# Optimization experiments

Hardware: AMD Instinct MI355X
Metric: run time of the kernel (lower is better)

The kernel has to match this reference:

```python
import jax, jax.numpy as jnp
import numpy as np
from math import sqrt

BATCH = 32
NUM_CLASSES = 81   # incl. background (class 0 skipped)
MAX_DET = 200      # max_output / per-class NMS candidate cap
IOU_T = 0.5        # criteria in decode_batch_with_nms_trace
CONF_T = 0.05      # score mask threshold


def make_dboxes():
    """Replicates dboxes_R34_coco([1200,1200]) -> (15130, 4) xywh, clipped to [0,1]."""
    fig = 1200
    feat = [50, 25, 13, 7, 3, 3]
    scales = [int(s * fig / 300) for s in [21, 45, 99, 153, 207, 261, 315]]
    ars = [[2], [2, 3], [2, 3], [2, 3], [2], [2]]
    boxes = []
    for idx, f in enumerate(feat):
        sk1 = scales[idx] / fig
        sk2 = scales[idx + 1] / fig
        sk3 = sqrt(sk1 * sk2)
        sizes = [(sk1, sk1), (sk3, sk3)]
        for a in ars[idx]:
            w, h = sk1 * sqrt(a), sk1 / sqrt(a)
            sizes += [(w, h), (h, w)]
        fk = fig // (fig // f)
        for (w, h) in sizes:
            for i in range(f):
                for j in range(f):
                    boxes.append(((j + 0.5) / fk, (i + 0.5) / fk, w, h))
    return np.clip(np.asarray(boxes, np.float32), 0.0, 1.0)


def setup_inputs() -> dict:
    key = jax.random.key(0)
    k1, k2 = jax.random.split(key)
    db = make_dboxes()                      # (15130, 4)
    N = db.shape[0]
    return {
        "bboxes_in": jax.random.normal(k1, (BATCH, 4, N), jnp.float32),
        "scores_in": jax.random.normal(k2, (BATCH, NUM_CLASSES, N), jnp.float32),
        "scale_xy": jnp.full((1,), 0.1, jnp.float32),
        "scale_wh": jnp.full((1,), 0.2, jnp.float32),
        "dboxes_xywh": jnp.asarray(db)[None],  # (1, N, 4)
    }


def _scale_back(bboxes_in, scores_in, scale_xy, scale_wh, dboxes_xywh):
    bb = jnp.transpose(bboxes_in, (0, 2, 1))          # (B, N, 4)
    sc = jnp.transpose(scores_in, (0, 2, 1))          # (B, N, L)
    d_xy, d_wh = dboxes_xywh[..., :2], dboxes_xywh[..., 2:]
    xy = bb[..., :2] * scale_xy * d_wh + d_xy
    wh = jnp.exp(bb[..., 2:] * scale_wh) * d_wh
    ltrb = jnp.concatenate([xy - 0.5 * wh, xy + 0.5 * wh], axis=-1)
    return ltrb, jax.nn.softmax(sc, axis=-1)


def _pairwise_iou(a, b):
    lt = jnp.maximum(a[:, None, :2], b[None, :, :2])
    rb = jnp.minimum(a[:, None, 2:], b[None, :, 2:])
    wh = jnp.clip(rb - lt, 0.0)
    inter = wh[..., 0] * wh[..., 1]
    area_a = (a[:, 2] - a[:, 0]) * (a[:, 3] - a[:, 1])
    area_b = (b[:, 2] - b[:, 0]) * (b[:, 3] - b[:, 1])
    return inter / (area_a[:, None] + area_b[None, :] - inter)


def _nms_one_class(boxes, cls_scores):
    """boxes (N,4), cls_scores (N,) -> (MAX_DET,4), (MAX_DET,) with suppressed = -1."""
    s = jnp.where(cls_scores > CONF_T, cls_scores, -1.0)   # mask score > 0.05
    top_s, idx = jax.lax.top_k(s, MAX_DET)                 # descending topk
    b = boxes[idx]
    iou = _pairwise_iou(b, b)                              # (K, K)
    valid = top_s > CONF_T

    def body(i, keep):  # greedy NMS over score-sorted candidates
        sup = (iou[i] > IOU_T) & keep[i] & (jnp.arange(MAX_DET) > i)
        return keep & ~sup

    keep = jax.lax.stop_gradient(jax.lax.fori_loop(0, MAX_DET, body, valid))
    return b, jnp.where(keep, top_s, -1.0)


def _decode(bboxes_in, scores_in, scale_xy, scale_wh, dboxes_xywh):
    boxes, probs = _scale_back(bboxes_in, scores_in, scale_xy, scale_wh, dboxes_xywh)
    cls_scores = jnp.transpose(probs[..., 1:], (0, 2, 1))   # (B, C=80, N); skip bg
    B, C = cls_scores.shape[0], cls_scores.shape[1]
    per_class = jax.vmap(_nms_one_class, in_axes=(None, 0))
    kb, ks = jax.vmap(per_class, in_axes=(0, 0))(boxes, cls_scores)  # (B,C,K,4),(B,C,K)
    labels = jnp.broadcast_to(
        jnp.arange(1, C + 1, dtype=jnp.int32)[:, None], (C, MAX_DET)).reshape(-1)
    kb = kb.reshape(B, C * MAX_DET, 4)
    ks = ks.reshape(B, C * MAX_DET)
    top_s, top_i = jax.lax.top_k(ks, MAX_DET)               # global top-200
    fb = jnp.take_along_axis(kb, top_i[..., None], axis=1)  # (B, 200, 4)
    fl = labels[top_i]                                      # (B, 200)
    valid = top_s > CONF_T
    return (fb * valid[..., None].astype(fb.dtype),
            jnp.where(valid, fl, 0),
            jnp.where(valid, top_s, 0.0))


def reference(bboxes_in, scores_in, scale_xy, scale_wh, dboxes_xywh):
    return _decode(bboxes_in, scores_in, scale_xy, scale_wh, dboxes_xywh)
```

## Files before the change

### kernel.cpp

```cpp
#include <hip/hip_runtime.h>
#include <stdint.h>

#define NPRIOR   15130
#define BATCH    32
#define NCLS     81
#define NCLS_OUT 80
#define NDET     200
#define CONF_T   0.05f
#define IOU_T    0.5f
#define CAND_CAP 1024
#define NGRP     5
#define GRP      16

__global__ __launch_bounds__(256) void zero_counters(unsigned int* __restrict__ counters, int n) {
    int i = blockIdx.x * 256 + threadIdx.x;
    if (i < n) counters[i] = 0u;
}

__global__ __launch_bounds__(256) void decode_softmax_scatter(
    const float* __restrict__ bboxes,
    const float* __restrict__ scores,
    const float* __restrict__ scale_xy_p,
    const float* __restrict__ scale_wh_p,
    const float* __restrict__ dboxes,
    float* __restrict__ boxes_ltrb,
    unsigned int* __restrict__ counters,
    unsigned long long* __restrict__ cand_g)
{
    int b = blockIdx.y;
    int n = blockIdx.x * 256 + threadIdx.x;
    if (n >= NPRIOR) return;

    float sx = scale_xy_p[0], sw = scale_wh_p[0];
    const float* bb = bboxes + (size_t)b * 4 * NPRIOR + n;
    float bx = bb[0];
    float by = bb[NPRIOR];
    float bw = bb[2 * NPRIOR];
    float bh = bb[3 * NPRIOR];
    float dx = dboxes[n * 4 + 0], dy = dboxes[n * 4 + 1];
    float dw = dboxes[n * 4 + 2], dh = dboxes[n * 4 + 3];
    float x = __fadd_rn(__fmul_rn(__fmul_rn(bx, sx), dw), dx);
    float y = __fadd_rn(__fmul_rn(__fmul_rn(by, sx), dh), dy);
    float w = __fmul_rn(expf(__fmul_rn(bw, sw)), dw);
    float h = __fmul_rn(expf(__fmul_rn(bh, sw)), dh);
    float hw = __fmul_rn(0.5f, w), hh = __fmul_rn(0.5f, h);
    float4 box;
    box.x = __fsub_rn(x, hw);
    box.y = __fsub_rn(y, hh);
    box.z = __fadd_rn(x, hw);
    box.w = __fadd_rn(y, hh);
    ((float4*)boxes_ltrb)[(size_t)b * NPRIOR + n] = box;

    const float* sc = scores + (size_t)b * NCLS * NPRIOR + n;
    float v[NCLS];
    float mx = -INFINITY;
#pragma unroll
    for (int c = 0; c < NCLS; ++c) {
        v[c] = sc[(size_t)c * NPRIOR];
        mx = fmaxf(mx, v[c]);
    }
    float sum = 0.f;
#pragma unroll
    for (int c = 0; c < NCLS; ++c) {
        v[c] = expf(__fsub_rn(v[c], mx));
        sum = __fadd_rn(sum, v[c]);
    }

    unsigned int invn = 0xFFFFFFFFu - (unsigned int)n;
#pragma unroll
    for (int c = 1; c < NCLS; ++c) {
        float p = __fdiv_rn(v[c], sum);
        if (p > CONF_T) {
            unsigned int idx = (unsigned int)b * NCLS_OUT + (unsigned int)(c - 1);
            unsigned int pos = atomicAdd(&counters[idx], 1u);
            if (pos < CAND_CAP) {
                cand_g[(size_t)idx * CAND_CAP + pos] =
                    ((unsigned long long)__float_as_uint(p) << 32) | (unsigned long long)invn;
            }
        }
    }
}

__device__ inline void bitonic_desc(unsigned long long* keys, int P, int tid) {
    for (int k = 2; k <= P; k <<= 1) {
        for (int j = k >> 1; j > 0; j >>= 1) {
            for (int i = tid; i < P; i += 256) {
                int l = i ^ j;
                if (l > i) {
                    unsigned long long a = keys[i], b = keys[l];
                    bool desc = ((i & k) == 0);
                    if (desc ? (a < b) : (a > b)) {
                        keys[i] = b;
                        keys[l] = a;
                    }
                }
            }
            __syncthreads();
        }
    }
}

__global__ __launch_bounds__(256) void nms_class(
    const unsigned int* __restrict__ counters,
    const unsigned long long* __restrict__ cand_g,
    const float* __restrict__ boxes_ltrb,
    float* __restrict__ cls_scores,
    float* __restrict__ cls_boxes)
{
    __shared__ unsigned long long cand[CAND_CAP];
    __shared__ float sbox[NDET][4];
    __shared__ float sscore[NDET];
    __shared__ unsigned long long rowm[NDET][4];
    __shared__ unsigned long long keepw[4];

    int tid = threadIdx.x;
    int b = blockIdx.y;
    int bc = b * NCLS_OUT + blockIdx.x;

    unsigned int cntu = counters[bc];
    int cnt = (cntu > CAND_CAP) ? CAND_CAP : (int)cntu;

    int P = 256;
    while (P < cnt) P <<= 1;

    for (int i = tid; i < P; i += 256)
        cand[i] = (i < cnt) ? cand_g[(size_t)bc * CAND_CAP + i] : 0ull;
    __syncthreads();

    bitonic_desc(cand, P, tid);

    int m = cnt < NDET ? cnt : NDET;
    if (tid < m) {
        unsigned long long key = cand[tid];
        unsigned int n = 0xFFFFFFFFu - (unsigned int)(key & 0xFFFFFFFFull);
        sscore[tid] = __uint_as_float((unsigned int)(key >> 32));
        float4 bx = ((const float4*)boxes_ltrb)[(size_t)b * NPRIOR + n];
        sbox[tid][0] = bx.x;
        sbox[tid][1] = bx.y;
        sbox[tid][2] = bx.z;
        sbox[tid][3] = bx.w;
    }
    __syncthreads();

    if (tid < m) {
        float l0 = sbox[tid][0], t0 = sbox[tid][1], r0 = sbox[tid][2], b0 = sbox[tid][3];
        float area0 = __fmul_rn(__fsub_rn(r0, l0), __fsub_rn(b0, t0));
        unsigned long long w0 = 0, w1 = 0, w2 = 0, w3 = 0;
        for (int j = tid + 1; j < m; ++j) {
            float lj = sbox[j][0], tj = sbox[j][1], rj = sbox[j][2], bj = sbox[j][3];
            float ltx = fmaxf(l0, lj), lty = fmaxf(t0, tj);
            float rbx = fminf(r0, rj), rby = fminf(b0, bj);
            float iw = fmaxf(__fsub_rn(rbx, ltx), 0.f);
            float ih = fmaxf(__fsub_rn(rby, lty), 0.f);
            float inter = __fmul_rn(iw, ih);
            float areaj = __fmul_rn(__fsub_rn(rj, lj), __fsub_rn(bj, tj));
            float den = __fsub_rn(__fadd_rn(area0, areaj), inter);
            float iou = __fdiv_rn(inter, den);
            if (iou > IOU_T) {
                if (j < 64) w0 |= 1ull << j;
                else if (j < 128) w1 |= 1ull << (j - 64);
                else if (j < 192) w2 |= 1ull << (j - 128);
                else w3 |= 1ull << (j - 192);
            }
        }
        rowm[tid][0] = w0;
        rowm[tid][1] = w1;
        rowm[tid][2] = w2;
        rowm[tid][3] = w3;
    }
    __syncthreads();

    if (tid == 0) {
        auto maskf = [](int t) -> unsigned long long {
            if (t <= 0) return 0ull;
            if (t >= 64) return ~0ull;
            return (1ull << t) - 1ull;
        };
        unsigned long long k0 = maskf(m), k1 = maskf(m - 64), k2 = maskf(m - 128), k3 = maskf(m - 192);
        for (int i = 0; i < m; ++i) {
            unsigned long long cur = (i < 64) ? k0 : (i < 128) ? k1 : (i < 192) ? k2 : k3;
            if ((cur >> (i & 63)) & 1ull) {
                k0 &= ~rowm[i][0];
                k1 &= ~rowm[i][1];
                k2 &= ~rowm[i][2];
                k3 &= ~rowm[i][3];
            }
        }
        keepw[0] = k0; keepw[1] = k1; keepw[2] = k2; keepw[3] = k3;
    }
    __syncthreads();

    if (tid < NDET) {
        float s = -1.0f;
        if (tid < m && ((keepw[tid >> 6] >> (tid & 63)) & 1ull)) s = sscore[tid];
        cls_scores[(size_t)bc * NDET + tid] = s;
        if (tid < m) {
            float4 bx;
            bx.x = sbox[tid][0]; bx.y = sbox[tid][1];
            bx.z = sbox[tid][2]; bx.w = sbox[tid][3];
            ((float4*)cls_boxes)[(size_t)bc * NDET + tid] = bx;
        }
    }
}

__global__ __launch_bounds__(256) void topk_group(
    const float* __restrict__ cls_scores,
    unsigned long long* __restrict__ grp_keys)
{
    __shared__ unsigned long long keys[4096];
    __shared__ unsigned int cnt_s;

    int tid = threadIdx.x;
    int g = blockIdx.x, b = blockIdx.y;
    if (tid == 0) cnt_s = 0;
    __syncthreads();

    int base_e = g * GRP * NDET;
    const float* sp = cls_scores + (size_t)b * NCLS_OUT * NDET + base_e;
    for (int i = tid; i < GRP * NDET; i += 256) {
        float s = sp[i];
        if (s > CONF_T) {
            unsigned int pos = atomicAdd(&cnt_s, 1u);
            unsigned int e = (unsigned int)(base_e + i);
            keys[pos] = ((unsigned long long)__float_as_uint(s) << 32) |
                        (unsigned long long)(0xFFFFFFFFu - e);
        }
    }
    __syncthreads();
    int cnt = (int)cnt_s;
    int P = 256;
    while (P < cnt) P <<= 1;
    for (int i = tid; i < P; i += 256)
        if (i >= cnt) keys[i] = 0ull;
    __syncthreads();

    bitonic_desc(keys, P, tid);

    if (tid < NDET)
        grp_keys[((size_t)b * NGRP + g) * NDET + tid] = (tid < cnt) ? keys[tid] : 0ull;
}

__global__ __launch_bounds__(256) void final_topk(
    const unsigned long long* __restrict__ grp_keys,
    const float* __restrict__ cls_boxes,
    float* __restrict__ out)
{
    __shared__ unsigned long long keys[1024];
    __shared__ unsigned int cnt_s;

    int tid = threadIdx.x, b = blockIdx.x;
    if (tid == 0) cnt_s = 0;
    __syncthreads();

    for (int i = tid; i < NGRP * NDET; i += 256) {
        unsigned long long k = grp_keys[(size_t)b * NGRP * NDET + i];
        if (k != 0ull) keys[atomicAdd(&cnt_s, 1u)] = k;
    }
    __syncthreads();
    int cnt = (int)cnt_s;
    int P = 256;
    while (P < cnt) P <<= 1;
    for (int i = tid; i < P; i += 256)
        if (i >= cnt) keys[i] = 0ull;
    __syncthreads();

    bitonic_desc(keys, P, tid);

    if (tid < NDET) {
        float4 bx = make_float4(0.f, 0.f, 0.f, 0.f);
        float lab = 0.f, sc = 0.f;
        if (tid < cnt) {
            unsigned long long k = keys[tid];
            unsigned int e = 0xFFFFFFFFu - (unsigned int)(k & 0xFFFFFFFFull);
            sc = __uint_as_float((unsigned int)(k >> 32));
            unsigned int c0 = e / NDET;
            bx = ((const float4*)cls_boxes)[(size_t)b * NCLS_OUT * NDET + e];
            lab = (float)(c0 + 1);
        }
        float* fb = out;
        float* fl = out + (size_t)BATCH * NDET * 4;
        float* fs = fl + (size_t)BATCH * NDET;
        ((float4*)fb)[b * NDET + tid] = bx;
        fl[b * NDET + tid] = lab;
        fs[b * NDET + tid] = sc;
    }
}

extern "C" void kernel_launch(void* const* d_in, const int* in_sizes, int n_in,
                              void* d_out, int out_size, void* d_ws, size_t ws_size,
                              hipStream_t stream) {
    const float* bboxes = (const float*)d_in[0];
    const float* scores = (const float*)d_in[1];
    const float* sxy    = (const float*)d_in[2];
    const float* swh    = (const float*)d_in[3];
    const float* dbx    = (const float*)d_in[4];
    float* out = (float*)d_out;

    char* ws = (char*)d_ws;
    size_t off = 0;
    auto alloc = [&](size_t bytes) -> char* {
        char* p = ws + off;
        off += (bytes + 255) & ~(size_t)255;
        return p;
    };
    float* boxes_ltrb            = (float*)alloc((size_t)BATCH * NPRIOR * 4 * 4);
    unsigned int* counters       = (unsigned int*)alloc((size_t)BATCH * NCLS_OUT * 4);
    unsigned long long* cand_g   = (unsigned long long*)alloc((size_t)BATCH * NCLS_OUT * CAND_CAP * 8);
    float* cls_scores            = (float*)alloc((size_t)BATCH * NCLS_OUT * NDET * 4);
    float* cls_boxes             = (float*)alloc((size_t)BATCH * NCLS_OUT * NDET * 4 * 4);
    unsigned long long* grp_keys = (unsigned long long*)alloc((size_t)BATCH * NGRP * NDET * 8);

    int ncounters = BATCH * NCLS_OUT;
    zero_counters<<<(ncounters + 255) / 256, 256, 0, stream>>>(counters, ncounters);

    dim3 gridA((NPRIOR + 255) / 256, BATCH);
    decode_softmax_scatter<<<gridA, 256, 0, stream>>>(
        bboxes, scores, sxy, swh, dbx, boxes_ltrb, counters, cand_g);

    dim3 gridB(NCLS_OUT, BATCH);
    nms_class<<<gridB, 256, 0, stream>>>(counters, cand_g, boxes_ltrb, cls_scores, cls_boxes);

    dim3 gridC1(NGRP, BATCH);
    topk_group<<<gridC1, 256, 0, stream>>>(cls_scores, grp_keys);

    final_topk<<<BATCH, 256, 0, stream>>>(grp_keys, cls_boxes, out);
}
```

Before: 799.0 us.

## Split decode into max/sum pass and scatter pass with four priors per thread

The single decode kernel held all 81 logits in registers, so each thread used many registers and few waves were resident. It is now split into two kernels. The first decodes boxes and writes the per-prior softmax max and sum. The second re-reads the scores, recomputes the probabilities and scatters candidates with atomics. Each thread now handles four priors using float2 loads, and zeroing the counters moves from its own launch into block 0 of the first kernel. The trade-off is reading the large score tensor three times instead of once, with one extra launch and a smaller grid.

```diff
diff --git a/kernel.cpp b/kernel.cpp
--- a/kernel.cpp
+++ b/kernel.cpp
@@ -11,71 +11,128 @@
 #define CAND_CAP 1024
 #define NGRP     5
 #define GRP      16
-
-__global__ __launch_bounds__(256) void zero_counters(unsigned int* __restrict__ counters, int n) {
-    int i = blockIdx.x * 256 + threadIdx.x;
-    if (i < n) counters[i] = 0u;
-}
-
-__global__ __launch_bounds__(256) void decode_softmax_scatter(
+#define NCNT     (BATCH * NCLS_OUT)
+
+__global__ __launch_bounds__(256) void decode_maxsum(
     const float* __restrict__ bboxes,
     const float* __restrict__ scores,
     const float* __restrict__ scale_xy_p,
     const float* __restrict__ scale_wh_p,
     const float* __restrict__ dboxes,
     float* __restrict__ boxes_ltrb,
+    float* __restrict__ maxsum,
+    unsigned int* __restrict__ counters)
+{
+    int tid = threadIdx.x;
+    if (blockIdx.x == 0 && blockIdx.y == 0) {
+        for (int i = tid; i < NCNT; i += 256) counters[i] = 0u;
+    }
+
+    int b = blockIdx.y;
+    int n0 = (blockIdx.x * 256 + tid) * 4;
+    if (n0 >= NPRIOR) return;
+    bool p1ok = (n0 + 3) < NPRIOR;
+
+    float sx = scale_xy_p[0], sw = scale_wh_p[0];
+
+    const float* bbb = bboxes + (size_t)b * 4 * NPRIOR;
+    float bx[4], by[4], bw[4], bh[4];
+#pragma unroll
+    for (int r = 0; r < 4; ++r) {
+        const float* row = bbb + (size_t)r * NPRIOR + n0;
+        float2 p0 = *(const float2*)row;
+        float2 p1 = p1ok ? *(const float2*)(row + 2) : make_float2(0.f, 0.f);
+        float* dst = (r == 0) ? bx : (r == 1) ? by : (r == 2) ? bw : bh;
+        dst[0] = p0.x; dst[1] = p0.y; dst[2] = p1.x; dst[3] = p1.y;
+    }
+#pragma unroll
+    for (int k = 0; k < 4; ++k) {
+        int n = n0 + k;
+        if (n >= NPRIOR) break;
+        float4 d = ((const float4*)dboxes)[n];
+        float x = __fadd_rn(__fmul_rn(__fmul_rn(bx[k], sx), d.z), d.x);
+        float y = __fadd_rn(__fmul_rn(__fmul_rn(by[k], sx), d.w), d.y);
+        float w = __fmul_rn(expf(__fmul_rn(bw[k], sw)), d.z);
+        float h = __fmul_rn(expf(__fmul_rn(bh[k], sw)), d.w);
+        float hw = __fmul_rn(0.5f, w), hh = __fmul_rn(0.5f, h);
+        float4 box;
+        box.x = __fsub_rn(x, hw);
+        box.y = __fsub_rn(y, hh);
+        box.z = __fadd_rn(x, hw);
+        box.w = __fadd_rn(y, hh);
+        ((float4*)boxes_ltrb)[(size_t)b * NPRIOR + n] = box;
+    }
+
+    const float* sc = scores + (size_t)b * NCLS * NPRIOR + n0;
+    float mx[4] = {-INFINITY, -INFINITY, -INFINITY, -INFINITY};
+#pragma unroll 3
+    for (int c = 0; c < NCLS; ++c) {
+        const float* p = sc + (size_t)c * NPRIOR;
+        float2 v0 = *(const float2*)p;
+        float2 v1 = p1ok ? *(const float2*)(p + 2) : make_float2(-INFINITY, -INFINITY);
+        mx[0] = fmaxf(mx[0], v0.x);
+        mx[1] = fmaxf(mx[1], v0.y);
+        mx[2] = fmaxf(mx[2], v1.x);
+        mx[3] = fmaxf(mx[3], v1.y);
+    }
+
+    float sm[4] = {0.f, 0.f, 0.f, 0.f};
+#pragma unroll 3
+    for (int c = 0; c < NCLS; ++c) {
+        const float* p = sc + (size_t)c * NPRIOR;
+        float2 v0 = *(const float2*)p;
+        float2 v1 = p1ok ? *(const float2*)(p + 2) : make_float2(0.f, 0.f);
+        sm[0] = __fadd_rn(sm[0], expf(__fsub_rn(v0.x, mx[0])));
+        sm[1] = __fadd_rn(sm[1], expf(__fsub_rn(v0.y, mx[1])));
+        sm[2] = __fadd_rn(sm[2], expf(__fsub_rn(v1.x, mx[2])));
+        sm[3] = __fadd_rn(sm[3], expf(__fsub_rn(v1.y, mx[3])));
+    }
+
+    float4 o0, o1;
+    o0.x = mx[0]; o0.y = sm[0]; o0.z = mx[1]; o0.w = sm[1];
+    o1.x = mx[2]; o1.y = sm[2]; o1.z = mx[3]; o1.w = sm[3];
+    float* msp = maxsum + ((size_t)b * NPRIOR + n0) * 2;
+    *(float4*)msp = o0;
+    if (p1ok) *(float4*)(msp + 4) = o1;
+}
+
+__global__ __launch_bounds__(256) void scatter_cand(
+    const float* __restrict__ scores,
+    const float* __restrict__ maxsum,
     unsigned int* __restrict__ counters,
     unsigned long long* __restrict__ cand_g)
 {
+    int tid = threadIdx.x;
     int b = blockIdx.y;
-    int n = blockIdx.x * 256 + threadIdx.x;
-    if (n >= NPRIOR) return;
-
-    float sx = scale_xy_p[0], sw = scale_wh_p[0];
-    const float* bb = bboxes + (size_t)b * 4 * NPRIOR + n;
-    float bx = bb[0];
-    float by = bb[NPRIOR];
-    float bw = bb[2 * NPRIOR];
-    float bh = bb[3 * NPRIOR];
-    float dx = dboxes[n * 4 + 0], dy = dboxes[n * 4 + 1];
-    float dw = dboxes[n * 4 + 2], dh = dboxes[n * 4 + 3];
-    float x = __fadd_rn(__fmul_rn(__fmul_rn(bx, sx), dw), dx);
-    float y = __fadd_rn(__fmul_rn(__fmul_rn(by, sx), dh), dy);
-    float w = __fmul_rn(expf(__fmul_rn(bw, sw)), dw);
-    float h = __fmul_rn(expf(__fmul_rn(bh, sw)), dh);
-    float hw = __fmul_rn(0.5f, w), hh = __fmul_rn(0.5f, h);
-    float4 box;
-    box.x = __fsub_rn(x, hw);
-    box.y = __fsub_rn(y, hh);
-    box.z = __fadd_rn(x, hw);
-    box.w = __fadd_rn(y, hh);
-    ((float4*)boxes_ltrb)[(size_t)b * NPRIOR + n] = box;
-
-    const float* sc = scores + (size_t)b * NCLS * NPRIOR + n;
-    float v[NCLS];
-    float mx = -INFINITY;
+    int n0 = (blockIdx.x * 256 + tid) * 4;
+    if (n0 >= NPRIOR) return;
+    bool p1ok = (n0 + 3) < NPRIOR;
+
+    const float* msp = maxsum + ((size_t)b * NPRIOR + n0) * 2;
+    float4 m0 = *(const float4*)msp;
+    float4 m1 = p1ok ? *(const float4*)(msp + 4) : make_float4(0.f, 1.f, 0.f, 1.f);
+    float mx[4] = {m0.x, m0.z, m1.x, m1.z};
+    float sm[4] = {m0.y, m0.w, m1.y, m1.w};
+
+    const float* sc = scores + (size_t)b * NCLS * NPRIOR + n0;
+    unsigned int cbase = (unsigned int)b * NCLS_OUT;
+
+    for (int c = 1; c < NCLS; ++c) {
+        const float* p = sc + (size_t)c * NPRIOR;
+        float2 v0 = *(const float2*)p;
+        float2 v1 = p1ok ? *(const float2*)(p + 2) : make_float2(-INFINITY, -INFINITY);
+        float v[4] = {v0.x, v0.y, v1.x, v1.y};
 #pragma unroll
-    for (int c = 0; c < NCLS; ++c) {
-        v[c] = sc[(size_t)c * NPRIOR];
-        mx = fmaxf(mx, v[c]);
-    }
-    float sum = 0.f;
-#pragma unroll
-    for (int c = 0; c < NCLS; ++c) {
-        v[c] = expf(__fsub_rn(v[c], mx));
-        sum = __fadd_rn(sum, v[c]);
-    }
-
-    unsigned int invn = 0xFFFFFFFFu - (unsigned int)n;
-#pragma unroll
-    for (int c = 1; c < NCLS; ++c) {
-        float p = __fdiv_rn(v[c], sum);
-        if (p > CONF_T) {
-            unsigned int idx = (unsigned int)b * NCLS_OUT + (unsigned int)(c - 1);
-            unsigned int pos = atomicAdd(&counters[idx], 1u);
-            if (pos < CAND_CAP) {
-                cand_g[(size_t)idx * CAND_CAP + pos] =
-                    ((unsigned long long)__float_as_uint(p) << 32) | (unsigned long long)invn;
+        for (int k = 0; k < 4; ++k) {
+            float pr = __fdiv_rn(expf(__fsub_rn(v[k], mx[k])), sm[k]);
+            if (pr > CONF_T) {
+                unsigned int idx = cbase + (unsigned int)(c - 1);
+                unsigned int pos = atomicAdd(&counters[idx], 1u);
+                if (pos < CAND_CAP) {
+                    cand_g[(size_t)idx * CAND_CAP + pos] =
+                        ((unsigned long long)__float_as_uint(pr) << 32) |
+                        (unsigned long long)(0xFFFFFFFFu - (unsigned int)(n0 + k));
+                }
             }
         }
     }
@@ -304,18 +361,18 @@
         return p;
     };
     float* boxes_ltrb            = (float*)alloc((size_t)BATCH * NPRIOR * 4 * 4);
-    unsigned int* counters       = (unsigned int*)alloc((size_t)BATCH * NCLS_OUT * 4);
-    unsigned long long* cand_g   = (unsigned long long*)alloc((size_t)BATCH * NCLS_OUT * CAND_CAP * 8);
+    float* maxsum                = (float*)alloc((size_t)BATCH * NPRIOR * 2 * 4);
+    unsigned int* counters       = (unsigned int*)alloc((size_t)NCNT * 4);
+    unsigned long long* cand_g   = (unsigned long long*)alloc((size_t)NCNT * CAND_CAP * 8);
     float* cls_scores            = (float*)alloc((size_t)BATCH * NCLS_OUT * NDET * 4);
     float* cls_boxes             = (float*)alloc((size_t)BATCH * NCLS_OUT * NDET * 4 * 4);
     unsigned long long* grp_keys = (unsigned long long*)alloc((size_t)BATCH * NGRP * NDET * 8);
 
-    int ncounters = BATCH * NCLS_OUT;
-    zero_counters<<<(ncounters + 255) / 256, 256, 0, stream>>>(counters, ncounters);
-
-    dim3 gridA((NPRIOR + 255) / 256, BATCH);
-    decode_softmax_scatter<<<gridA, 256, 0, stream>>>(
-        bboxes, scores, sxy, swh, dbx, boxes_ltrb, counters, cand_g);
+    dim3 gridA((NPRIOR + 1023) / 1024, BATCH);
+    decode_maxsum<<<gridA, 256, 0, stream>>>(
+        bboxes, scores, sxy, swh, dbx, boxes_ltrb, maxsum, counters);
+
+    scatter_cand<<<gridA, 256, 0, stream>>>(scores, maxsum, counters, cand_g);
 
     dim3 gridB(NCLS_OUT, BATCH);
     nms_class<<<gridB, 256, 0, stream>>>(counters, cand_g, boxes_ltrb, cls_scores, cls_boxes);
```

After: 800.2 us. Within noise of the previous version (+0.2%).

## Stage softmax scores in shared memory and parallelize class scatter across threads

Applied to the files above, without the earlier changes.

The decode/softmax kernel now loads a 128-prior by 81-class tile of logits into shared memory. It computes per-prior max and sum with one thread per prior, then spreads the per-class probability and threshold scatter over all 256 threads. This avoids holding 81 values in registers per thread, which cuts register pressure and raises occupancy, and it splits the serial per-thread class loop across more threads. The zero-counter kernel is replaced by hipMemsetAsync and dboxes are read as a single float4. In exchange the exponentials are recomputed in the scatter phase and the block uses about 41 KB of shared memory, which may limit occupancy.

```diff
diff --git a/kernel.cpp b/kernel.cpp
--- a/kernel.cpp
+++ b/kernel.cpp
@@ -11,13 +11,10 @@
 #define CAND_CAP 1024
 #define NGRP     5
 #define GRP      16
-
-__global__ __launch_bounds__(256) void zero_counters(unsigned int* __restrict__ counters, int n) {
-    int i = blockIdx.x * 256 + threadIdx.x;
-    if (i < n) counters[i] = 0u;
-}
-
-__global__ __launch_bounds__(256) void decode_softmax_scatter(
+#define NCNT     (BATCH * NCLS_OUT)
+#define TP       128
+
+__global__ __launch_bounds__(256) void fused_decode_scatter(
     const float* __restrict__ bboxes,
     const float* __restrict__ scores,
     const float* __restrict__ scale_xy_p,
@@ -27,55 +24,78 @@
     unsigned int* __restrict__ counters,
     unsigned long long* __restrict__ cand_g)
 {
+    __shared__ float sv[NCLS * TP];
+    __shared__ float smx[TP];
+    __shared__ float ssum[TP];
+
+    int tid = threadIdx.x;
     int b = blockIdx.y;
-    int n = blockIdx.x * 256 + threadIdx.x;
-    if (n >= NPRIOR) return;
-
-    float sx = scale_xy_p[0], sw = scale_wh_p[0];
-    const float* bb = bboxes + (size_t)b * 4 * NPRIOR + n;
-    float bx = bb[0];
-    float by = bb[NPRIOR];
-    float bw = bb[2 * NPRIOR];
-    float bh = bb[3 * NPRIOR];
-    float dx = dboxes[n * 4 + 0], dy = dboxes[n * 4 + 1];
-    float dw = dboxes[n * 4 + 2], dh = dboxes[n * 4 + 3];
-    float x = __fadd_rn(__fmul_rn(__fmul_rn(bx, sx), dw), dx);
-    float y = __fadd_rn(__fmul_rn(__fmul_rn(by, sx), dh), dy);
-    float w = __fmul_rn(expf(__fmul_rn(bw, sw)), dw);
-    float h = __fmul_rn(expf(__fmul_rn(bh, sw)), dh);
-    float hw = __fmul_rn(0.5f, w), hh = __fmul_rn(0.5f, h);
-    float4 box;
-    box.x = __fsub_rn(x, hw);
-    box.y = __fsub_rn(y, hh);
-    box.z = __fadd_rn(x, hw);
-    box.w = __fadd_rn(y, hh);
-    ((float4*)boxes_ltrb)[(size_t)b * NPRIOR + n] = box;
-
-    const float* sc = scores + (size_t)b * NCLS * NPRIOR + n;
-    float v[NCLS];
-    float mx = -INFINITY;
-#pragma unroll
-    for (int c = 0; c < NCLS; ++c) {
-        v[c] = sc[(size_t)c * NPRIOR];
-        mx = fmaxf(mx, v[c]);
-    }
-    float sum = 0.f;
-#pragma unroll
-    for (int c = 0; c < NCLS; ++c) {
-        v[c] = expf(__fsub_rn(v[c], mx));
-        sum = __fadd_rn(sum, v[c]);
-    }
-
-    unsigned int invn = 0xFFFFFFFFu - (unsigned int)n;
-#pragma unroll
-    for (int c = 1; c < NCLS; ++c) {
-        float p = __fdiv_rn(v[c], sum);
-        if (p > CONF_T) {
+    int n0 = blockIdx.x * TP;
+    int nvalid = NPRIOR - n0;
+    if (nvalid > TP) nvalid = TP;
+
+    const float* sb = scores + (size_t)b * NCLS * NPRIOR + n0;
+    if (nvalid == TP) {
+        for (int i = tid; i < NCLS * TP; i += 256) {
+            int c = i >> 7, p = i & (TP - 1);
+            sv[i] = sb[(size_t)c * NPRIOR + p];
+        }
+    } else {
+        for (int i = tid; i < NCLS * TP; i += 256) {
+            int c = i >> 7, p = i & (TP - 1);
+            sv[i] = (p < nvalid) ? sb[(size_t)c * NPRIOR + p] : 0.f;
+        }
+    }
+
+    if (tid < nvalid) {
+        int n = n0 + tid;
+        float sx = scale_xy_p[0], sw = scale_wh_p[0];
+        const float* bbb = bboxes + (size_t)b * 4 * NPRIOR + n;
+        float bx = bbb[0];
+        float by = bbb[NPRIOR];
+        float bw = bbb[2 * NPRIOR];
+        float bh = bbb[3 * NPRIOR];
+        float4 d = ((const float4*)dboxes)[n];
+        float x = __fadd_rn(__fmul_rn(__fmul_rn(bx, sx), d.z), d.x);
+        float y = __fadd_rn(__fmul_rn(__fmul_rn(by, sx), d.w), d.y);
+        float w = __fmul_rn(expf(__fmul_rn(bw, sw)), d.z);
+        float h = __fmul_rn(expf(__fmul_rn(bh, sw)), d.w);
+        float hw = __fmul_rn(0.5f, w), hh = __fmul_rn(0.5f, h);
+        float4 box;
+        box.x = __fsub_rn(x, hw);
+        box.y = __fsub_rn(y, hh);
+        box.z = __fadd_rn(x, hw);
+        box.w = __fadd_rn(y, hh);
+        ((float4*)boxes_ltrb)[(size_t)b * NPRIOR + n] = box;
+    }
+    __syncthreads();
+
+    if (tid < nvalid) {
+        float mx = -INFINITY;
+#pragma unroll 9
+        for (int c = 0; c < NCLS; ++c)
+            mx = fmaxf(mx, sv[c * TP + tid]);
+        float sm = 0.f;
+#pragma unroll 9
+        for (int c = 0; c < NCLS; ++c)
+            sm = __fadd_rn(sm, expf(__fsub_rn(sv[c * TP + tid], mx)));
+        smx[tid] = mx;
+        ssum[tid] = sm;
+    }
+    __syncthreads();
+
+    for (int i = tid; i < NCLS_OUT * TP; i += 256) {
+        int c = (i >> 7) + 1;
+        int p = i & (TP - 1);
+        if (p >= nvalid) continue;
+        float pr = __fdiv_rn(expf(__fsub_rn(sv[c * TP + p], smx[p])), ssum[p]);
+        if (pr > CONF_T) {
             unsigned int idx = (unsigned int)b * NCLS_OUT + (unsigned int)(c - 1);
             unsigned int pos = atomicAdd(&counters[idx], 1u);
             if (pos < CAND_CAP) {
                 cand_g[(size_t)idx * CAND_CAP + pos] =
-                    ((unsigned long long)__float_as_uint(p) << 32) | (unsigned long long)invn;
+                    ((unsigned long long)__float_as_uint(pr) << 32) |
+                    (unsigned long long)(0xFFFFFFFFu - (unsigned int)(n0 + p));
             }
         }
     }
@@ -304,17 +324,16 @@
         return p;
     };
     float* boxes_ltrb            = (float*)alloc((size_t)BATCH * NPRIOR * 4 * 4);
-    unsigned int* counters       = (unsigned int*)alloc((size_t)BATCH * NCLS_OUT * 4);
-    unsigned long long* cand_g   = (unsigned long long*)alloc((size_t)BATCH * NCLS_OUT * CAND_CAP * 8);
+    unsigned int* counters       = (unsigned int*)alloc((size_t)NCNT * 4);
+    unsigned long long* cand_g   = (unsigned long long*)alloc((size_t)NCNT * CAND_CAP * 8);
     float* cls_scores            = (float*)alloc((size_t)BATCH * NCLS_OUT * NDET * 4);
     float* cls_boxes             = (float*)alloc((size_t)BATCH * NCLS_OUT * NDET * 4 * 4);
     unsigned long long* grp_keys = (unsigned long long*)alloc((size_t)BATCH * NGRP * NDET * 8);
 
-    int ncounters = BATCH * NCLS_OUT;
-    zero_counters<<<(ncounters + 255) / 256, 256, 0, stream>>>(counters, ncounters);
-
-    dim3 gridA((NPRIOR + 255) / 256, BATCH);
-    decode_softmax_scatter<<<gridA, 256, 0, stream>>>(
+    hipMemsetAsync(counters, 0, (size_t)NCNT * 4, stream);
+
+    dim3 gridA((NPRIOR + TP - 1) / TP, BATCH);
+    fused_decode_scatter<<<gridA, 256, 0, stream>>>(
         bboxes, scores, sxy, swh, dbx, boxes_ltrb, counters, cand_g);
 
     dim3 gridB(NCLS_OUT, BATCH);
```

Measured after the change: 1.421 ms. 1.78x slower.
